# Performance work log

Measured on AMD Instinct MI355X. Metric: run time of the kernel, lower is better.

Reference implementation:

```python
import jax, jax.numpy as jnp
import numpy as np

EPS = 1e-5

def _lrelu(x):
    return jnp.where(x >= 0, x, 0.2 * x)

def _bn(x, g, b):
    # train-mode BatchNorm2d over (B, N, k) per channel (channel-last layout)
    m = x.mean((0, 1, 2), keepdims=True)
    v = x.var((0, 1, 2), keepdims=True)  # biased variance, as torch uses for normalization
    return (x - m) * jax.lax.rsqrt(v + EPS) * g + b

def _knn(pos, k):
    # pos: (B, 3, N); negative squared euclidean distance, top-k = k nearest (incl. self)
    inner = -2.0 * jnp.einsum('bcn,bcm->bnm', pos, pos)
    xx = jnp.sum(pos * pos, axis=1)  # (B, N)
    pd = -xx[:, :, None] - inner - xx[:, None, :]  # (B, N, N)
    return jax.lax.top_k(pd, k)[1]  # (B, N, k) int32

def _edge(xt, idx):
    # xt: (B, N, C), idx: (B, N, k) -> (B, N, k, 2C) = [neighbor - center, center]
    nb = jax.vmap(lambda f, i: f[i])(xt, idx)  # (B, N, k, C) gather
    ctr = jnp.broadcast_to(xt[:, :, None, :], nb.shape)
    return jnp.concatenate([nb - ctr, ctr], axis=-1)

def _conv_bn_lrelu(h, W, g, b):
    # 1x1 conv as einsum on channel-last (B, N, k, Cin) -> (B, N, k, Cout)
    return _lrelu(_bn(jnp.einsum('bnkc,oc->bnko', h, W), g, b))

def _forward(x, k, W1, g1, b1, W2, g2, b2, W3, g3, b3, W4, g4, b4, W5, g5, b5, W9a, b9a, W9b, b9b):
    xt = x.transpose(0, 2, 1)  # (B, N, 67)
    idx = _knn(x[:, -3:, :], k)  # knn on xyz coords (dim9=True)
    h = _conv_bn_lrelu(_edge(xt, idx), W1, g1, b1)
    h = _conv_bn_lrelu(h, W2, g2, b2)
    x1 = h.max(axis=2)  # (B, N, 64) max over k neighbors
    h = _conv_bn_lrelu(_edge(x1, idx), W3, g3, b3)
    h = _conv_bn_lrelu(h, W4, g4, b4)
    x2 = h.max(axis=2)
    x3 = _conv_bn_lrelu(_edge(x2, idx), W5, g5, b5).max(axis=2)
    f = jnp.concatenate([x1, x2, x3], axis=-1)  # (B, N, 192)
    h = jax.nn.relu(jnp.einsum('bnc,oc->bno', f, W9a) + b9a)
    out = jnp.einsum('bnc,oc->bno', h, W9b) + b9b  # (B, N, 16)
    return out.transpose(0, 2, 1)  # (B, 16, N) to match torch layout

def setup_inputs() -> dict:
    key = jax.random.key(0)
    ks = jax.random.split(key, 8)
    B, C, N, K = 1, 67, 8192, 20
    s = 0.1
    return {
        'x': jax.random.normal(ks[0], (B, C, N), jnp.float32),
        'k': K,
        'W1': jax.random.normal(ks[1], (64, 134), jnp.float32) * s,
        'g1': jnp.ones((64,), jnp.float32), 'b1': jnp.zeros((64,), jnp.float32),
        'W2': jax.random.normal(ks[2], (64, 64), jnp.float32) * s,
        'g2': jnp.ones((64,), jnp.float32), 'b2': jnp.zeros((64,), jnp.float32),
        'W3': jax.random.normal(ks[3], (64, 128), jnp.float32) * s,
        'g3': jnp.ones((64,), jnp.float32), 'b3': jnp.zeros((64,), jnp.float32),
        'W4': jax.random.normal(ks[4], (64, 64), jnp.float32) * s,
        'g4': jnp.ones((64,), jnp.float32), 'b4': jnp.zeros((64,), jnp.float32),
        'W5': jax.random.normal(ks[5], (64, 128), jnp.float32) * s,
        'g5': jnp.ones((64,), jnp.float32), 'b5': jnp.zeros((64,), jnp.float32),
        'W9a': jax.random.normal(ks[6], (128, 192), jnp.float32) * s,
        'b9a': jnp.zeros((128,), jnp.float32),
        'W9b': jax.random.normal(ks[7], (16, 128), jnp.float32) * s,
        'b9b': jnp.zeros((16,), jnp.float32),
    }

def reference(x, k, W1, g1, b1, W2, g2, b2, W3, g3, b3, W4, g4, b4, W5, g5, b5, W9a, b9a, W9b, b9b):
    return _forward(x, k, W1, g1, b1, W2, g2, b2, W3, g3, b3, W4, g4, b4, W5, g5, b5, W9a, b9a, W9b, b9b)
```

## Files before the change

### kernel.cpp

```cpp
#include <hip/hip_runtime.h>

#define NPTS 8192
#define KNN  20
#define NREP 64
#define NSLICE 8
#define SLICE 1024
#define CAP 256
#define THSUB 2048

__device__ __forceinline__ float pair_dist4(float qx, float qy, float qz, float xxn, float4 c) {
    float dot = fmaf(qz, c.z, fmaf(qy, c.y, qx * c.x));
    return fmaf(2.f, dot, -xxn) - c.w;
}
__device__ __forceinline__ float self_sq(float dx, float dy, float dz) {
    return fmaf(dz, dz, fmaf(dy, dy, dx * dx));
}
__device__ __forceinline__ float lrelu(float v) { return (v >= 0.f) ? v : 0.2f * v; }

__device__ __forceinline__ void compute_affine(const float* __restrict__ gs,
                                               const float* __restrict__ g,
                                               const float* __restrict__ b,
                                               float* saff, int tid) {
    if (tid < 64) {
        float s = 0.f, ss = 0.f;
        for (int r = 0; r < NREP; ++r) { s += gs[r * 128 + tid]; ss += gs[r * 128 + 64 + tid]; }
        const float invM = 1.f / (float)(NPTS * KNN);
        float mean = s * invM;
        float var = ss * invM - mean * mean;
        float sc = g[tid] * rsqrtf(var + 1e-5f);
        saff[tid] = sc;
        saff[64 + tid] = b[tid] - mean * sc;
    }
}

__global__ __launch_bounds__(256) void prep_kernel(const float* __restrict__ x,
                                                   const float* __restrict__ W1,
                                                   const float* __restrict__ W3,
                                                   const float* __restrict__ W5,
                                                   const float* __restrict__ W9a,
                                                   const float* __restrict__ W9b,
                                                   float4* __restrict__ pk,
                                                   float* __restrict__ Wt1,
                                                   float* __restrict__ Wt3,
                                                   float* __restrict__ Wt5,
                                                   float* __restrict__ W9at,
                                                   float* __restrict__ W9bt,
                                                   float* __restrict__ gsAll,
                                                   int* __restrict__ scount) {
    int gid = blockIdx.x * 256 + threadIdx.x;
    if (gid < NPTS) {
        float dx = x[64 * NPTS + gid], dy = x[65 * NPTS + gid], dz = x[66 * NPTS + gid];
        pk[gid] = make_float4(dx, dy, dz, self_sq(dx, dy, dz));
        return;
    }
    gid -= NPTS;
    if (gid < 67 * 128) {
        int c = gid >> 7, o = gid & 127;
        Wt1[gid] = (o < 64) ? W1[o * 134 + c] : W1[(o - 64) * 134 + 67 + c];
        return;
    }
    gid -= 67 * 128;
    if (gid < 64 * 128) {
        int c = gid >> 7, o = gid & 127;
        Wt3[gid] = (o < 64) ? W3[o * 128 + c] : W3[(o - 64) * 128 + 64 + c];
        return;
    }
    gid -= 64 * 128;
    if (gid < 64 * 128) {
        int c = gid >> 7, o = gid & 127;
        Wt5[gid] = (o < 64) ? W5[o * 128 + c] : W5[(o - 64) * 128 + 64 + c];
        return;
    }
    gid -= 64 * 128;
    if (gid < 192 * 128) {
        int c = gid >> 7, j = gid & 127;
        W9at[gid] = W9a[j * 192 + c];
        return;
    }
    gid -= 192 * 128;
    if (gid < 128 * 16) {
        int c = gid >> 4, j = gid & 15;
        W9bt[gid] = W9b[j * 128 + c];
        return;
    }
    gid -= 128 * 16;
    if (gid < 5 * NREP * 128) { gsAll[gid] = 0.f; return; }
    gid -= 5 * NREP * 128;
    if (gid < NPTS) scount[gid] = 0;
}

__global__ __launch_bounds__(256) void knn_theta_proj(const float4* __restrict__ pk,
                                                      float* __restrict__ theta,
                                                      const float* __restrict__ X,
                                                      const float* __restrict__ Wt1,
                                                      float* __restrict__ P) {
    __shared__ float4 cpt[THSUB];
    int tid = threadIdx.x;
    if (blockIdx.x >= 512) {
        int bb = blockIdx.x - 512;
        int o = tid & 127, h = tid >> 7;
        int n0 = bb * 8 + h * 4;
        float acc[4] = {0.f, 0.f, 0.f, 0.f};
        for (int c = 0; c < 67; ++c) {
            float w = Wt1[c * 128 + o];
#pragma unroll
            for (int i = 0; i < 4; ++i) acc[i] = fmaf(X[(n0 + i) + c * NPTS], w, acc[i]);
        }
#pragma unroll
        for (int i = 0; i < 4; ++i) P[(n0 + i) * 128 + o] = acc[i];
        return;
    }
    int wid = tid >> 6, lane = tid & 63;
    int qbase = blockIdx.x * 16 + wid * 4;
    for (int i = tid; i < THSUB; i += 256) cpt[i] = pk[i];
    float qx[4], qy[4], qz[4], xxn[4], mv[4];
#pragma unroll
    for (int qi = 0; qi < 4; ++qi) {
        float4 qp = pk[qbase + qi];
        qx[qi] = qp.x; qy[qi] = qp.y; qz[qi] = qp.z; xxn[qi] = qp.w;
        mv[qi] = -INFINITY;
    }
    __syncthreads();
    for (int t = 0; t < THSUB / 64; ++t) {
        float4 c = cpt[t * 64 + lane];
#pragma unroll
        for (int qi = 0; qi < 4; ++qi)
            mv[qi] = fmaxf(mv[qi], pair_dist4(qx[qi], qy[qi], qz[qi], xxn[qi], c));
    }
#pragma unroll 1
    for (int qi = 0; qi < 4; ++qi) {
        float sel = mv[qi];
        float th = -INFINITY;
        for (int r = 0; r < KNN; ++r) {
            float v = sel;
#pragma unroll
            for (int m = 32; m >= 1; m >>= 1) v = fmaxf(v, __shfl_xor(v, m));
            th = v;
            unsigned long long bm = __ballot(sel == v);
            if (lane == __ffsll(bm) - 1) sel = -INFINITY;
        }
        if (lane == 0) theta[qbase + qi] = th - 1e-3f;
    }
}

__global__ __launch_bounds__(256) void knn_filter(const float4* __restrict__ pk,
                                                  const float* __restrict__ theta,
                                                  int* __restrict__ scount,
                                                  int2* __restrict__ surv) {
    __shared__ float4 cpt[SLICE];
    int tid = threadIdx.x, wid = tid >> 6, lane = tid & 63;
    int qg = blockIdx.x >> 3;
    int s  = blockIdx.x & 7;
    for (int i = tid; i < SLICE; i += 256) cpt[i] = pk[s * SLICE + i];
    int qbase = qg * 16 + wid * 4;
    float qx[4], qy[4], qz[4], xxn[4], th[4];
#pragma unroll
    for (int qi = 0; qi < 4; ++qi) {
        float4 qp = pk[qbase + qi];
        qx[qi] = qp.x; qy[qi] = qp.y; qz[qi] = qp.z; xxn[qi] = qp.w;
        th[qi] = theta[qbase + qi];
    }
    __syncthreads();
    for (int t = 0; t < SLICE / 64; ++t) {
        int gi = s * SLICE + t * 64 + lane;
        float4 c = cpt[t * 64 + lane];
#pragma unroll
        for (int qi = 0; qi < 4; ++qi) {
            float d = pair_dist4(qx[qi], qy[qi], qz[qi], xxn[qi], c);
            bool p = (d >= th[qi]);
            unsigned long long mk = __ballot(p);
            if (mk) {
                int q = qbase + qi;
                int src = __ffsll(mk) - 1;
                int base = 0;
                if (lane == src) base = atomicAdd(&scount[q], (int)__popcll(mk));
                base = __shfl(base, src);
                if (p) {
                    int pos = base + (int)__popcll(mk & ((1ull << lane) - 1));
                    if (pos < CAP) surv[q * CAP + pos] = make_int2(__float_as_int(d), gi);
                }
            }
        }
    }
}

__global__ __launch_bounds__(256) void knn_select_zsum(const float4* __restrict__ pk,
                                                       const int* __restrict__ scount,
                                                       const int2* __restrict__ surv,
                                                       int* __restrict__ idx_out,
                                                       const float* __restrict__ P,
                                                       float* __restrict__ gs) {
    int tid = threadIdx.x, wid = tid >> 6, lane = tid & 63;
    int q = blockIdx.x * 4 + wid;
    int cnt = scount[q];
    int mi_keep = 0;
    if (cnt <= CAP) {
        float sv[4]; int si[4];
#pragma unroll
        for (int r = 0; r < 4; ++r) {
            int j = r * 64 + lane;
            bool ok = j < cnt;
            int2 pr = ok ? surv[q * CAP + j] : make_int2(0, 0);
            sv[r] = ok ? __int_as_float(pr.x) : -INFINITY;
            si[r] = ok ? pr.y : 0x7fffffff;
        }
        for (int r = 0; r < KNN; ++r) {
            float lv = -INFINITY; int li = 0x7fffffff; int ls = -1;
#pragma unroll
            for (int s3 = 0; s3 < 4; ++s3) {
                bool g = (sv[s3] > lv) || (sv[s3] == lv && si[s3] < li);
                if (g) { lv = sv[s3]; li = si[s3]; ls = s3; }
            }
            float wv = lv; int wi = li;
#pragma unroll
            for (int m = 32; m >= 1; m >>= 1) {
                float ov = __shfl_xor(wv, m); int oi = __shfl_xor(wi, m);
                if (ov > wv || (ov == wv && oi < wi)) { wv = ov; wi = oi; }
            }
            if (lv == wv && li == wi) {
#pragma unroll
                for (int s3 = 0; s3 < 4; ++s3)
                    if (s3 == ls) { sv[s3] = -INFINITY; si[s3] = 0x7fffffff; }
            }
            if (lane == 0) idx_out[q * KNN + r] = wi;
            if (lane == r) mi_keep = wi;
        }
    } else {
        float4 qp = pk[q];
        float qx = qp.x, qy = qp.y, qz = qp.z, xxn = qp.w;
        float pv = INFINITY; int pi = -1;
        for (int r = 0; r < KNN; ++r) {
            float bv = -INFINITY; int bi = 0x7fffffff;
            for (int t = 0; t < NPTS / 64; ++t) {
                int i = t * 64 + lane;
                float d = pair_dist4(qx, qy, qz, xxn, pk[i]);
                bool adm = (d < pv) || (d == pv && i > pi);
                if (adm && (d > bv || (d == bv && i < bi))) { bv = d; bi = i; }
            }
            float wv = bv; int wi = bi;
#pragma unroll
            for (int m = 32; m >= 1; m >>= 1) {
                float ov = __shfl_xor(wv, m); int oi = __shfl_xor(wi, m);
                if (ov > wv || (ov == wv && oi < wi)) { wv = ov; wi = oi; }
            }
            if (lane == 0) idx_out[q * KNN + r] = wi;
            if (lane == r) mi_keep = wi;
            pv = wv; pi = wi;
        }
    }
    float An = P[q * 128 + lane];
    float Bn = P[q * 128 + 64 + lane];
    float base = Bn - An;
    float sum = 0.f, ss = 0.f;
#pragma unroll
    for (int kk = 0; kk < KNN; ++kk) {
        int m = __shfl(mi_keep, kk);
        float z = P[(size_t)m * 128 + lane] + base;
        sum += z;
        ss = fmaf(z, z, ss);
    }
    float* gg = gs + (blockIdx.x & (NREP - 1)) * 128;
    atomicAdd(gg + lane, sum);
    atomicAdd(gg + 64 + lane, ss);
}

__global__ __launch_bounds__(256) void zsum_kernel(const float* __restrict__ P,
                                                   const int* __restrict__ idx,
                                                   float* __restrict__ gs) {
    int tid = threadIdx.x;
    int o = tid & 63;
    float sum = 0.f, sumsq = 0.f;
    int n0 = blockIdx.x * 4;
#pragma unroll
    for (int ni = 0; ni < 4; ++ni) {
        int n = n0 + ni;
        float An = P[n * 128 + o];
        float Bn = P[n * 128 + 64 + o];
        float base = Bn - An;
#pragma unroll
        for (int kk2 = 0; kk2 < 5; ++kk2) {
            int kk = (tid >> 6) + kk2 * 4;
            int m = idx[n * KNN + kk];
            float z = P[m * 128 + o] + base;
            sum += z;
            sumsq = fmaf(z, z, sumsq);
        }
    }
    __shared__ float s1[256], s2[256];
    s1[tid] = sum; s2[tid] = sumsq;
    __syncthreads();
    if (tid < 64) {
        float a = s1[tid] + s1[tid + 64] + s1[tid + 128] + s1[tid + 192];
        float b = s2[tid] + s2[tid + 64] + s2[tid + 128] + s2[tid + 192];
        float* g = gs + (blockIdx.x & (NREP - 1)) * 128;
        atomicAdd(g + tid, a);
        atomicAdd(g + 64 + tid, b);
    }
}

__global__ __launch_bounds__(256) void conv_gemm_kernel(const float* __restrict__ P,
                                                        const int* __restrict__ idx,
                                                        const float* __restrict__ gsIn,
                                                        const float* __restrict__ gIn,
                                                        const float* __restrict__ bIn,
                                                        const float* __restrict__ W,
                                                        float* __restrict__ gsOut,
                                                        float* __restrict__ Mx,
                                                        float* __restrict__ Mn) {
    __shared__ float As[80][68];
    __shared__ float Ws[64][68];
    __shared__ float saff[128];
    int tid = threadIdx.x;
    int r0 = blockIdx.x * 80;

    compute_affine(gsIn, gIn, bIn, saff, tid);
    for (int i2 = tid; i2 < 1024; i2 += 256) {
        int rr = i2 >> 4, c4 = (i2 & 15) * 4;
        *(float4*)&Ws[rr][c4] = *(const float4*)&W[rr * 64 + c4];
    }
    __syncthreads();

#pragma unroll 5
    for (int i2 = tid; i2 < 1280; i2 += 256) {
        int rr = i2 >> 4, c4 = (i2 & 15) * 4;
        int grow = r0 + rr;
        int n = grow / 20;
        int m = idx[grow];
        float4 zn = *(const float4*)&P[(size_t)m * 128 + c4];
        float4 an = *(const float4*)&P[(size_t)n * 128 + c4];
        float4 bn = *(const float4*)&P[(size_t)n * 128 + 64 + c4];
        float4 ov; float z;
        z = zn.x + (bn.x - an.x); ov.x = lrelu(fmaf(z, saff[c4 + 0], saff[64 + c4 + 0]));
        z = zn.y + (bn.y - an.y); ov.y = lrelu(fmaf(z, saff[c4 + 1], saff[64 + c4 + 1]));
        z = zn.z + (bn.z - an.z); ov.z = lrelu(fmaf(z, saff[c4 + 2], saff[64 + c4 + 2]));
        z = zn.w + (bn.w - an.w); ov.w = lrelu(fmaf(z, saff[c4 + 3], saff[64 + c4 + 3]));
        *(float4*)&As[rr][c4] = ov;
    }
    __syncthreads();

    int ty = tid >> 4, tx = tid & 15;
    float acc[5][4];
#pragma unroll
    for (int i = 0; i < 5; ++i)
#pragma unroll
        for (int j = 0; j < 4; ++j) acc[i][j] = 0.f;

    for (int c4 = 0; c4 < 64; c4 += 4) {
        float4 a4[5], w4[4];
#pragma unroll
        for (int i = 0; i < 5; ++i) a4[i] = *(const float4*)&As[ty + 16 * i][c4];
#pragma unroll
        for (int j = 0; j < 4; ++j) w4[j] = *(const float4*)&Ws[tx + 16 * j][c4];
#pragma unroll
        for (int i = 0; i < 5; ++i)
#pragma unroll
            for (int j = 0; j < 4; ++j) {
                acc[i][j] = fmaf(a4[i].x, w4[j].x, acc[i][j]);
                acc[i][j] = fmaf(a4[i].y, w4[j].y, acc[i][j]);
                acc[i][j] = fmaf(a4[i].z, w4[j].z, acc[i][j]);
                acc[i][j] = fmaf(a4[i].w, w4[j].w, acc[i][j]);
            }
    }
    __syncthreads();

#pragma unroll
    for (int i = 0; i < 5; ++i)
#pragma unroll
        for (int j = 0; j < 4; ++j) As[ty + 16 * i][tx + 16 * j] = acc[i][j];
    __syncthreads();

    int a = tid >> 6, o = tid & 63;
    float mxv = -INFINITY, mnv = INFINITY, s = 0.f, ss = 0.f;
#pragma unroll
    for (int r = 0; r < 20; ++r) {
        float v = As[20 * a + r][o];
        mxv = fmaxf(mxv, v); mnv = fminf(mnv, v);
        s += v; ss = fmaf(v, v, ss);
    }
    int n = blockIdx.x * 4 + a;
    Mx[n * 64 + o] = mxv;
    Mn[n * 64 + o] = mnv;
    float* sred = &Ws[0][0];
    float* ssred = sred + 256;
    sred[a * 64 + o] = s;
    ssred[a * 64 + o] = ss;
    __syncthreads();
    if (tid < 64) {
        float ts = sred[tid] + sred[64 + tid] + sred[128 + tid] + sred[192 + tid];
        float tss = ssred[tid] + ssred[64 + tid] + ssred[128 + tid] + ssred[192 + tid];
        float* gg = gsOut + (blockIdx.x & (NREP - 1)) * 128;
        atomicAdd(gg + tid, ts);
        atomicAdd(gg + 64 + tid, tss);
    }
}

__global__ __launch_bounds__(256) void pool_proj_kernel(const float* __restrict__ Mx,
                                                        const float* __restrict__ Mn,
                                                        const float* __restrict__ gsIn,
                                                        const float* __restrict__ g,
                                                        const float* __restrict__ b,
                                                        const float* __restrict__ Wt,
                                                        float* __restrict__ Xout,
                                                        float* __restrict__ Pout) {
    __shared__ float saff[128];
    __shared__ float xs[4][64];
    int tid = threadIdx.x;
    compute_affine(gsIn, g, b, saff, tid);
    __syncthreads();
    int n0 = blockIdx.x * 4;
    int pp = tid >> 6, o = tid & 63;
    float sc = saff[o], sh = saff[64 + o];
    float v = (sc >= 0.f) ? Mx[(n0 + pp) * 64 + o] : Mn[(n0 + pp) * 64 + o];
    float xv = lrelu(fmaf(v, sc, sh));
    Xout[(n0 + pp) * 64 + o] = xv;
    xs[pp][o] = xv;
    __syncthreads();
    int o2 = tid & 127, h = tid >> 7;
    int p0 = h * 2, p1 = h * 2 + 1;
    float a0 = 0.f, a1 = 0.f;
    for (int c = 0; c < 64; ++c) {
        float w = Wt[c * 128 + o2];
        a0 = fmaf(xs[p0][c], w, a0);
        a1 = fmaf(xs[p1][c], w, a1);
    }
    Pout[(n0 + p0) * 128 + o2] = a0;
    Pout[(n0 + p1) * 128 + o2] = a1;
}

__global__ __launch_bounds__(256) void zpool_kernel(const float* __restrict__ P,
                                                    const int* __restrict__ idx,
                                                    const float* __restrict__ gsIn,
                                                    const float* __restrict__ g,
                                                    const float* __restrict__ b,
                                                    float* __restrict__ Xout) {
    __shared__ float saff[128];
    int tid = threadIdx.x;
    compute_affine(gsIn, g, b, saff, tid);
    __syncthreads();
    int gid = blockIdx.x * 256 + tid;
    int n = gid >> 6, o = gid & 63;
    float An = P[n * 128 + o];
    float Bn = P[n * 128 + 64 + o];
    float base = Bn - An;
    float mxz = -INFINITY, mnz = INFINITY;
#pragma unroll
    for (int kk = 0; kk < KNN; ++kk) {
        int m = idx[n * KNN + kk];
        float z = P[m * 128 + o] + base;
        mxz = fmaxf(mxz, z); mnz = fminf(mnz, z);
    }
    float sc = saff[o], sh = saff[64 + o];
    float v = (sc >= 0.f) ? mxz : mnz;
    Xout[gid] = lrelu(fmaf(v, sc, sh));
}

__global__ __launch_bounds__(128) void mlp_kernel(const float* __restrict__ x1,
                                                  const float* __restrict__ x2,
                                                  const float* __restrict__ x3,
                                                  const float* __restrict__ W9at,
                                                  const float* __restrict__ b9a,
                                                  const float* __restrict__ W9bt,
                                                  const float* __restrict__ b9b,
                                                  float* __restrict__ out) {
    __shared__ float hs[8][128];
    int tid = threadIdx.x;
    int j = tid;
    int n0 = blockIdx.x * 8;
    float acc[8];
    float bj = b9a[j];
#pragma unroll
    for (int p = 0; p < 8; ++p) acc[p] = bj;
    for (int c = 0; c < 64; ++c) {
        float w = W9at[c * 128 + j];
#pragma unroll
        for (int p = 0; p < 8; ++p) acc[p] = fmaf(x1[(n0 + p) * 64 + c], w, acc[p]);
    }
    for (int c = 0; c < 64; ++c) {
        float w = W9at[(64 + c) * 128 + j];
#pragma unroll
        for (int p = 0; p < 8; ++p) acc[p] = fmaf(x2[(n0 + p) * 64 + c], w, acc[p]);
    }
    for (int c = 0; c < 64; ++c) {
        float w = W9at[(128 + c) * 128 + j];
#pragma unroll
        for (int p = 0; p < 8; ++p) acc[p] = fmaf(x3[(n0 + p) * 64 + c], w, acc[p]);
    }
#pragma unroll
    for (int p = 0; p < 8; ++p) hs[p][j] = fmaxf(acc[p], 0.f);
    __syncthreads();
    int p2 = tid >> 4, j2 = tid & 15;
    float a = b9b[j2];
    for (int c = 0; c < 128; ++c) a = fmaf(hs[p2][c], W9bt[c * 16 + j2], a);
    out[j2 * NPTS + n0 + p2] = a;
}

extern "C" void kernel_launch(void* const* d_in, const int* in_sizes, int n_in,
                              void* d_out, int out_size, void* d_ws, size_t ws_size,
                              hipStream_t stream) {
    const float* x   = (const float*)d_in[0];
    const float* W1  = (const float*)d_in[2];
    const float* g1  = (const float*)d_in[3];
    const float* b1  = (const float*)d_in[4];
    const float* W2  = (const float*)d_in[5];
    const float* g2  = (const float*)d_in[6];
    const float* b2  = (const float*)d_in[7];
    const float* W3  = (const float*)d_in[8];
    const float* g3  = (const float*)d_in[9];
    const float* b3  = (const float*)d_in[10];
    const float* W4  = (const float*)d_in[11];
    const float* g4  = (const float*)d_in[12];
    const float* b4  = (const float*)d_in[13];
    const float* W5  = (const float*)d_in[14];
    const float* g5  = (const float*)d_in[15];
    const float* b5  = (const float*)d_in[16];
    const float* W9a = (const float*)d_in[17];
    const float* b9a = (const float*)d_in[18];
    const float* W9b = (const float*)d_in[19];
    const float* b9b = (const float*)d_in[20];
    float* out = (float*)d_out;

    char* ws = (char*)d_ws;
    int*    idx    = (int*)(ws + 0);
    float4* pk     = (float4*)(ws + 655360);
    float*  P      = (float*)(ws + 786432);
    float*  Mx     = (float*)(ws + 4980736);
    float*  Mn     = (float*)(ws + 7077888);
    float*  gsAll  = (float*)(ws + 9175040);
    float*  x1b    = (float*)(ws + 9338880);
    float*  x2b    = (float*)(ws + 11436032);
    float*  x3b    = (float*)(ws + 13533184);
    float*  Wt1    = (float*)(ws + 15630336);
    float*  Wt3    = (float*)(ws + 15664640);
    float*  Wt5    = (float*)(ws + 15697408);
    float*  W9at   = (float*)(ws + 15730176);
    float*  W9bt   = (float*)(ws + 15828480);
    float*  theta  = (float*)(ws + 15836672);
    int*    scount = (int*)(ws + 15869440);
    int2*   surv   = (int2*)(ws + 15902208);
    (void)ws_size; (void)in_sizes; (void)n_in; (void)out_size;

    float* gs1 = gsAll;
    float* gs2 = gsAll + 1 * NREP * 128;
    float* gs3 = gsAll + 2 * NREP * 128;
    float* gs4 = gsAll + 3 * NREP * 128;
    float* gs5 = gsAll + 4 * NREP * 128;

    prep_kernel<<<426, 256, 0, stream>>>(x, W1, W3, W5, W9a, W9b, pk, Wt1, Wt3, Wt5, W9at, W9bt, gsAll, scount);
    knn_theta_proj<<<1536, 256, 0, stream>>>(pk, theta, x, Wt1, P);
    knn_filter<<<(NPTS / 16) * NSLICE, 256, 0, stream>>>(pk, theta, scount, surv);
    knn_select_zsum<<<NPTS / 4, 256, 0, stream>>>(pk, scount, surv, idx, P, gs1);

    conv_gemm_kernel<<<NPTS * KNN / 80, 256, 0, stream>>>(P, idx, gs1, g1, b1, W2, gs2, Mx, Mn);
    pool_proj_kernel<<<NPTS / 4, 256, 0, stream>>>(Mx, Mn, gs2, g2, b2, Wt3, x1b, P);

    zsum_kernel<<<NPTS / 4, 256, 0, stream>>>(P, idx, gs3);
    conv_gemm_kernel<<<NPTS * KNN / 80, 256, 0, stream>>>(P, idx, gs3, g3, b3, W4, gs4, Mx, Mn);
    pool_proj_kernel<<<NPTS / 4, 256, 0, stream>>>(Mx, Mn, gs4, g4, b4, Wt5, x2b, P);

    zsum_kernel<<<NPTS / 4, 256, 0, stream>>>(P, idx, gs5);
    zpool_kernel<<<NPTS * 64 / 256, 256, 0, stream>>>(P, idx, gs5, g5, b5, x3b);

    mlp_kernel<<<NPTS / 8, 128, 0, stream>>>(x1b, x2b, x3b, W9at, b9a, W9bt, b9b, out);
}
```

Baseline: 260.6 us.

## Fuse KNN filter and selection into one kernel with shared-memory candidate buffers

Merges the knn_filter and knn_select_zsum kernels into a single knn_fsel kernel. Each block handles 8 queries, scans all points in 1024-point LDS chunks, and keeps survivor indices in shared memory instead of a global surv/scount buffer. Distances are recomputed at selection time. This removes a kernel launch, the global atomics and the survivor round trip through memory, and the scount zeroing in prep. The cost is lower parallelism, since each block now scans all 8192 points sequentially in one of 1024 blocks. The smaller cap of 160 also sends more queries to the slow brute-force fallback.

```diff
diff --git a/kernel.cpp b/kernel.cpp
--- a/kernel.cpp
+++ b/kernel.cpp
@@ -3,10 +3,8 @@
 #define NPTS 8192
 #define KNN  20
 #define NREP 64
-#define NSLICE 8
-#define SLICE 1024
-#define CAP 256
 #define THSUB 2048
+#define FCAP 160
 
 __device__ __forceinline__ float pair_dist4(float qx, float qy, float qz, float xxn, float4 c) {
     float dot = fmaf(qz, c.z, fmaf(qy, c.y, qx * c.x));
@@ -45,8 +43,7 @@
                                                    float* __restrict__ Wt5,
                                                    float* __restrict__ W9at,
                                                    float* __restrict__ W9bt,
-                                                   float* __restrict__ gsAll,
-                                                   int* __restrict__ scount) {
+                                                   float* __restrict__ gsAll) {
     int gid = blockIdx.x * 256 + threadIdx.x;
     if (gid < NPTS) {
         float dx = x[64 * NPTS + gid], dy = x[65 * NPTS + gid], dz = x[66 * NPTS + gid];
@@ -84,9 +81,7 @@
         return;
     }
     gid -= 128 * 16;
-    if (gid < 5 * NREP * 128) { gsAll[gid] = 0.f; return; }
-    gid -= 5 * NREP * 128;
-    if (gid < NPTS) scount[gid] = 0;
+    if (gid < 5 * NREP * 128) gsAll[gid] = 0.f;
 }
 
 __global__ __launch_bounds__(256) void knn_theta_proj(const float4* __restrict__ pk,
@@ -143,125 +138,127 @@
     }
 }
 
-__global__ __launch_bounds__(256) void knn_filter(const float4* __restrict__ pk,
-                                                  const float* __restrict__ theta,
-                                                  int* __restrict__ scount,
-                                                  int2* __restrict__ surv) {
-    __shared__ float4 cpt[SLICE];
+__global__ __launch_bounds__(256) void knn_fsel(const float4* __restrict__ pk,
+                                                const float* __restrict__ theta,
+                                                int* __restrict__ idx_out,
+                                                const float* __restrict__ P,
+                                                float* __restrict__ gs) {
+    __shared__ float4 cpt[1024];
+    __shared__ int bufi[8][FCAP];
+    __shared__ int scnt[8];
     int tid = threadIdx.x, wid = tid >> 6, lane = tid & 63;
-    int qg = blockIdx.x >> 3;
-    int s  = blockIdx.x & 7;
-    for (int i = tid; i < SLICE; i += 256) cpt[i] = pk[s * SLICE + i];
-    int qbase = qg * 16 + wid * 4;
-    float qx[4], qy[4], qz[4], xxn[4], th[4];
-#pragma unroll
-    for (int qi = 0; qi < 4; ++qi) {
-        float4 qp = pk[qbase + qi];
-        qx[qi] = qp.x; qy[qi] = qp.y; qz[qi] = qp.z; xxn[qi] = qp.w;
-        th[qi] = theta[qbase + qi];
-    }
-    __syncthreads();
-    for (int t = 0; t < SLICE / 64; ++t) {
-        int gi = s * SLICE + t * 64 + lane;
-        float4 c = cpt[t * 64 + lane];
-#pragma unroll
-        for (int qi = 0; qi < 4; ++qi) {
-            float d = pair_dist4(qx[qi], qy[qi], qz[qi], xxn[qi], c);
-            bool p = (d >= th[qi]);
-            unsigned long long mk = __ballot(p);
-            if (mk) {
-                int q = qbase + qi;
-                int src = __ffsll(mk) - 1;
+    int qbase = blockIdx.x * 8;
+    int q0 = qbase + wid * 2, q1 = q0 + 1;
+    if (tid < 8) scnt[tid] = 0;
+    float4 qa = pk[q0], qb = pk[q1];
+    float tha = theta[q0], thb = theta[q1];
+
+    for (int ch = 0; ch < 8; ++ch) {
+        __syncthreads();
+        for (int i = tid; i < 1024; i += 256) cpt[i] = pk[ch * 1024 + i];
+        __syncthreads();
+        for (int t = 0; t < 16; ++t) {
+            int gi = ch * 1024 + t * 64 + lane;
+            float4 c = cpt[t * 64 + lane];
+            float d0 = pair_dist4(qa.x, qa.y, qa.z, qa.w, c);
+            bool p0 = (d0 >= tha);
+            unsigned long long m0 = __ballot(p0);
+            if (m0) {
+                int src = __ffsll(m0) - 1;
                 int base = 0;
-                if (lane == src) base = atomicAdd(&scount[q], (int)__popcll(mk));
+                if (lane == src) base = atomicAdd(&scnt[wid * 2], (int)__popcll(m0));
                 base = __shfl(base, src);
-                if (p) {
-                    int pos = base + (int)__popcll(mk & ((1ull << lane) - 1));
-                    if (pos < CAP) surv[q * CAP + pos] = make_int2(__float_as_int(d), gi);
-                }
+                int pos = base + (int)__popcll(m0 & ((1ull << lane) - 1));
+                if (p0 && pos < FCAP) bufi[wid * 2][pos] = gi;
+            }
+            float d1 = pair_dist4(qb.x, qb.y, qb.z, qb.w, c);
+            bool p1 = (d1 >= thb);
+            unsigned long long m1 = __ballot(p1);
+            if (m1) {
+                int src = __ffsll(m1) - 1;
+                int base = 0;
+                if (lane == src) base = atomicAdd(&scnt[wid * 2 + 1], (int)__popcll(m1));
+                base = __shfl(base, src);
+                int pos = base + (int)__popcll(m1 & ((1ull << lane) - 1));
+                if (p1 && pos < FCAP) bufi[wid * 2 + 1][pos] = gi;
             }
         }
     }
-}
-
-__global__ __launch_bounds__(256) void knn_select_zsum(const float4* __restrict__ pk,
-                                                       const int* __restrict__ scount,
-                                                       const int2* __restrict__ surv,
-                                                       int* __restrict__ idx_out,
-                                                       const float* __restrict__ P,
-                                                       float* __restrict__ gs) {
-    int tid = threadIdx.x, wid = tid >> 6, lane = tid & 63;
-    int q = blockIdx.x * 4 + wid;
-    int cnt = scount[q];
-    int mi_keep = 0;
-    if (cnt <= CAP) {
-        float sv[4]; int si[4];
-#pragma unroll
-        for (int r = 0; r < 4; ++r) {
-            int j = r * 64 + lane;
-            bool ok = j < cnt;
-            int2 pr = ok ? surv[q * CAP + j] : make_int2(0, 0);
-            sv[r] = ok ? __int_as_float(pr.x) : -INFINITY;
-            si[r] = ok ? pr.y : 0x7fffffff;
+    __syncthreads();
+
+#pragma unroll 1
+    for (int qi = 0; qi < 2; ++qi) {
+        int q = q0 + qi;
+        float4 qp = (qi == 0) ? qa : qb;
+        int cnt = scnt[wid * 2 + qi];
+        int mi_keep = 0;
+        if (cnt <= FCAP) {
+            float sv[3]; int si[3];
+#pragma unroll
+            for (int r = 0; r < 3; ++r) {
+                int j = r * 64 + lane;
+                bool ok = j < cnt;
+                int sidx = ok ? bufi[wid * 2 + qi][j] : 0x7fffffff;
+                float dv = ok ? pair_dist4(qp.x, qp.y, qp.z, qp.w, pk[sidx]) : -INFINITY;
+                sv[r] = dv; si[r] = sidx;
+            }
+            for (int r = 0; r < KNN; ++r) {
+                float lv = -INFINITY; int li = 0x7fffffff; int ls = -1;
+#pragma unroll
+                for (int s3 = 0; s3 < 3; ++s3) {
+                    bool g = (sv[s3] > lv) || (sv[s3] == lv && si[s3] < li);
+                    if (g) { lv = sv[s3]; li = si[s3]; ls = s3; }
+                }
+                float wv = lv; int wi = li;
+#pragma unroll
+                for (int m = 32; m >= 1; m >>= 1) {
+                    float ov = __shfl_xor(wv, m); int oi = __shfl_xor(wi, m);
+                    if (ov > wv || (ov == wv && oi < wi)) { wv = ov; wi = oi; }
+                }
+                if (lv == wv && li == wi) {
+#pragma unroll
+                    for (int s3 = 0; s3 < 3; ++s3)
+                        if (s3 == ls) { sv[s3] = -INFINITY; si[s3] = 0x7fffffff; }
+                }
+                if (lane == 0) idx_out[q * KNN + r] = wi;
+                if (lane == r) mi_keep = wi;
+            }
+        } else {
+            float pv = INFINITY; int pi = -1;
+            for (int r = 0; r < KNN; ++r) {
+                float bv = -INFINITY; int bi = 0x7fffffff;
+                for (int t = 0; t < NPTS / 64; ++t) {
+                    int i = t * 64 + lane;
+                    float d = pair_dist4(qp.x, qp.y, qp.z, qp.w, pk[i]);
+                    bool adm = (d < pv) || (d == pv && i > pi);
+                    if (adm && (d > bv || (d == bv && i < bi))) { bv = d; bi = i; }
+                }
+                float wv = bv; int wi = bi;
+#pragma unroll
+                for (int m = 32; m >= 1; m >>= 1) {
+                    float ov = __shfl_xor(wv, m); int oi = __shfl_xor(wi, m);
+                    if (ov > wv || (ov == wv && oi < wi)) { wv = ov; wi = oi; }
+                }
+                if (lane == 0) idx_out[q * KNN + r] = wi;
+                if (lane == r) mi_keep = wi;
+                pv = wv; pi = wi;
+            }
         }
-        for (int r = 0; r < KNN; ++r) {
-            float lv = -INFINITY; int li = 0x7fffffff; int ls = -1;
-#pragma unroll
-            for (int s3 = 0; s3 < 4; ++s3) {
-                bool g = (sv[s3] > lv) || (sv[s3] == lv && si[s3] < li);
-                if (g) { lv = sv[s3]; li = si[s3]; ls = s3; }
-            }
-            float wv = lv; int wi = li;
-#pragma unroll
-            for (int m = 32; m >= 1; m >>= 1) {
-                float ov = __shfl_xor(wv, m); int oi = __shfl_xor(wi, m);
-                if (ov > wv || (ov == wv && oi < wi)) { wv = ov; wi = oi; }
-            }
-            if (lv == wv && li == wi) {
-#pragma unroll
-                for (int s3 = 0; s3 < 4; ++s3)
-                    if (s3 == ls) { sv[s3] = -INFINITY; si[s3] = 0x7fffffff; }
-            }
-            if (lane == 0) idx_out[q * KNN + r] = wi;
-            if (lane == r) mi_keep = wi;
+        float An = P[q * 128 + lane];
+        float Bn = P[q * 128 + 64 + lane];
+        float base = Bn - An;
+        float sum = 0.f, ss = 0.f;
+#pragma unroll
+        for (int kk = 0; kk < KNN; ++kk) {
+            int m = __shfl(mi_keep, kk);
+            float z = P[(size_t)m * 128 + lane] + base;
+            sum += z;
+            ss = fmaf(z, z, ss);
         }
-    } else {
-        float4 qp = pk[q];
-        float qx = qp.x, qy = qp.y, qz = qp.z, xxn = qp.w;
-        float pv = INFINITY; int pi = -1;
-        for (int r = 0; r < KNN; ++r) {
-            float bv = -INFINITY; int bi = 0x7fffffff;
-            for (int t = 0; t < NPTS / 64; ++t) {
-                int i = t * 64 + lane;
-                float d = pair_dist4(qx, qy, qz, xxn, pk[i]);
-                bool adm = (d < pv) || (d == pv && i > pi);
-                if (adm && (d > bv || (d == bv && i < bi))) { bv = d; bi = i; }
-            }
-            float wv = bv; int wi = bi;
-#pragma unroll
-            for (int m = 32; m >= 1; m >>= 1) {
-                float ov = __shfl_xor(wv, m); int oi = __shfl_xor(wi, m);
-                if (ov > wv || (ov == wv && oi < wi)) { wv = ov; wi = oi; }
-            }
-            if (lane == 0) idx_out[q * KNN + r] = wi;
-            if (lane == r) mi_keep = wi;
-            pv = wv; pi = wi;
-        }
-    }
-    float An = P[q * 128 + lane];
-    float Bn = P[q * 128 + 64 + lane];
-    float base = Bn - An;
-    float sum = 0.f, ss = 0.f;
-#pragma unroll
-    for (int kk = 0; kk < KNN; ++kk) {
-        int m = __shfl(mi_keep, kk);
-        float z = P[(size_t)m * 128 + lane] + base;
-        sum += z;
-        ss = fmaf(z, z, ss);
-    }
-    float* gg = gs + (blockIdx.x & (NREP - 1)) * 128;
-    atomicAdd(gg + lane, sum);
-    atomicAdd(gg + 64 + lane, ss);
+        float* gg = gs + (blockIdx.x & (NREP - 1)) * 128;
+        atomicAdd(gg + lane, sum);
+        atomicAdd(gg + 64 + lane, ss);
+    }
 }
 
 __global__ __launch_bounds__(256) void zsum_kernel(const float* __restrict__ P,
@@ -535,8 +532,6 @@
     float*  W9at   = (float*)(ws + 15730176);
     float*  W9bt   = (float*)(ws + 15828480);
     float*  theta  = (float*)(ws + 15836672);
-    int*    scount = (int*)(ws + 15869440);
-    int2*   surv   = (int2*)(ws + 15902208);
     (void)ws_size; (void)in_sizes; (void)n_in; (void)out_size;
 
     float* gs1 = gsAll;
@@ -545,10 +540,9 @@
     float* gs4 = gsAll + 3 * NREP * 128;
     float* gs5 = gsAll + 4 * NREP * 128;
 
-    prep_kernel<<<426, 256, 0, stream>>>(x, W1, W3, W5, W9a, W9b, pk, Wt1, Wt3, Wt5, W9at, W9bt, gsAll, scount);
+    prep_kernel<<<394, 256, 0, stream>>>(x, W1, W3, W5, W9a, W9b, pk, Wt1, Wt3, Wt5, W9at, W9bt, gsAll);
     knn_theta_proj<<<1536, 256, 0, stream>>>(pk, theta, x, Wt1, P);
-    knn_filter<<<(NPTS / 16) * NSLICE, 256, 0, stream>>>(pk, theta, scount, surv);
-    knn_select_zsum<<<NPTS / 4, 256, 0, stream>>>(pk, scount, surv, idx, P, gs1);
+    knn_fsel<<<NPTS / 8, 256, 0, stream>>>(pk, theta, idx, P, gs1);
 
     conv_gemm_kernel<<<NPTS * KNN / 80, 256, 0, stream>>>(P, idx, gs1, g1, b1, W2, gs2, Mx, Mn);
     pool_proj_kernel<<<NPTS / 4, 256, 0, stream>>>(Mx, Mn, gs2, g2, b2, Wt3, x1b, P);
```

Result: slower. 764.4 us (+193.3%).
